# Kernel tuning notes

Measured on AMD Instinct MI355X. Metric: run time of the kernel, lower is better.

Reference implementation:

```python
import jax, jax.numpy as jnp
import numpy as np

N_NODES = 100000
N_EDGES = 1600000
C_IN, C_HID, C_OUT = 128, 64, 32


def setup_inputs() -> dict:
    key = jax.random.key(0)
    kx, ke, kw1, kw2 = jax.random.split(key, 4)
    x = jax.random.normal(kx, (N_NODES, C_IN), dtype=jnp.float32)
    edge_index = jax.random.randint(ke, (2, N_EDGES), 0, N_NODES, dtype=jnp.int64)
    # Glorot-ish init for the two GCNConv linear weights; PyG GCNConv bias inits to zero.
    W1 = jax.random.normal(kw1, (C_IN, C_HID), dtype=jnp.float32) / np.sqrt(C_IN)
    b1 = jnp.zeros((C_HID,), dtype=jnp.float32)
    W2 = jax.random.normal(kw2, (C_HID, C_OUT), dtype=jnp.float32) / np.sqrt(C_HID)
    b2 = jnp.zeros((C_OUT,), dtype=jnp.float32)
    return {"x": x, "edge_index": edge_index, "W1": W1, "b1": b1, "W2": W2, "b2": b2}


def _gcn_conv(x, W, b, src, dst, num_nodes):
    """PyG GCNConv: add self-loops, symmetric norm D^-1/2 A D^-1/2, linear, aggregate, bias."""
    xw = x @ W  # [N, out]
    # degree at destination, including the self-loop contribution of 1 per node
    deg = jnp.zeros((num_nodes,), xw.dtype).at[dst].add(1.0) + 1.0
    dinv = jax.lax.rsqrt(deg)  # deg >= 1 thanks to self-loops
    norm = dinv[src] * dinv[dst]  # [E]
    # scatter-add messages from source nodes into destination nodes
    out = jnp.zeros_like(xw).at[dst].add(norm[:, None] * xw[src])
    # self-loop term: norm_ii = dinv[i]^2
    out = out + (dinv * dinv)[:, None] * xw
    return out + b


def reference(x, edge_index, W1, b1, W2, b2):
    src, dst = edge_index[0], edge_index[1]
    h = _gcn_conv(x, W1, b1, src, dst, N_NODES)
    h = jax.nn.relu(h)
    # Dropout(0.1) is identity in eval mode (deterministic reference)
    out = _gcn_conv(h, W2, b2, src, dst, N_NODES)
    return out
```

## Files before the change

### kernel.cpp

```cpp
#include <hip/hip_runtime.h>
#include <hip/hip_bf16.h>


#define C_IN  128
#define C_HID 64
#define C_OUT 32
#define BK_SHIFT 10
#define BK_NODES (1 << BK_SHIFT)
#define BK_MAXB  128
#define EPB 2048

typedef unsigned short ushort_t;
typedef __attribute__((ext_vector_type(8))) short bf16x8;
typedef __attribute__((ext_vector_type(4))) float f32x4;

__device__ inline ushort_t f2bf(float f) {
    __hip_bfloat16 b = __float2bfloat16(f);
    return *reinterpret_cast<ushort_t*>(&b);
}
__device__ inline float bflo(unsigned int v) { return __uint_as_float(v << 16); }
__device__ inline float bfhi(unsigned int v) { return __uint_as_float(v & 0xffff0000u); }


__global__ void zero_bcur(int* __restrict__ bcur, int nb) {
    int i = threadIdx.x;
    if (i < nb) bcur[i] = 0;
}

__global__ __launch_bounds__(256) void bucket_edges(
        const int* __restrict__ src, const int* __restrict__ dst,
        int* __restrict__ bcur, unsigned int* __restrict__ bucketed,
        int cap, int E, int nb) {
    __shared__ unsigned int stage[EPB];
    __shared__ unsigned char bkt[EPB];
    __shared__ int cnt[BK_MAXB];
    __shared__ int lofs[BK_MAXB];
    __shared__ int base[BK_MAXB];
    int tid = threadIdx.x;
    for (int i = tid; i < nb; i += 256) cnt[i] = 0;
    __syncthreads();
    int e0 = blockIdx.x * EPB;
    int myb[8]; int myr[8]; unsigned int mys[8];
    #pragma unroll
    for (int i = 0; i < 8; ++i) {
        int e = e0 + i * 256 + tid;
        if (e < E) {
            int d = dst[e];
            int s = src[e];
            int b = d >> BK_SHIFT;
            myb[i] = b;
            mys[i] = (unsigned int)s | ((unsigned int)(d & (BK_NODES - 1)) << 17);
            myr[i] = atomicAdd(&cnt[b], 1);
        } else myb[i] = -1;
    }
    __syncthreads();
    if (tid < 64) {
        int b0 = 2 * tid, b1 = 2 * tid + 1;
        int c0 = (b0 < nb) ? cnt[b0] : 0;
        int c1 = (b1 < nb) ? cnt[b1] : 0;
        int p = c0 + c1;
        int s = p;
        #pragma unroll
        for (int off = 1; off < 64; off <<= 1) {
            int t = __shfl_up(s, off, 64);
            if (tid >= off) s += t;
        }
        if (b0 < nb) lofs[b0] = s - p;
        if (b1 < nb) lofs[b1] = s - c1;
    }
    __syncthreads();
    #pragma unroll
    for (int i = 0; i < 8; ++i) {
        if (myb[i] >= 0) {
            int p = lofs[myb[i]] + myr[i];
            stage[p] = mys[i];
            bkt[p] = (unsigned char)myb[i];
        }
    }
    for (int i = tid; i < nb; i += 256)
        base[i] = atomicAdd(&bcur[i], cnt[i]);
    __syncthreads();
    int total = min(EPB, E - e0);
    for (int p = tid; p < total; p += 256) {
        int b = bkt[p];
        int di = base[b] + (p - lofs[b]);
        if (di < cap)
            bucketed[(size_t)b * cap + di] = stage[p];
    }
}

__global__ __launch_bounds__(1024) void fill_csr_fused(
        const unsigned int* __restrict__ bucketed, const int* __restrict__ bcur,
        int* __restrict__ offsets, float* __restrict__ dinv,
        int* __restrict__ csr_src, int cap, int nb, int n) {
    __shared__ int hist[BK_NODES];
    __shared__ int wsum[16];
    __shared__ int sEb[BK_MAXB + 1];
    __shared__ int sW[2];
    int tid = threadIdx.x, lane = tid & 63, wid = tid >> 6;
    int b = blockIdx.x;
    int v128 = 0, s128 = 0;
    if (tid < 128) {
        v128 = (tid < nb) ? min(bcur[tid], cap) : 0;
        s128 = v128;
        #pragma unroll
        for (int off = 1; off < 64; off <<= 1) {
            int t = __shfl_up(s128, off, 64);
            if (lane >= off) s128 += t;
        }
        if (lane == 63) sW[wid] = s128;
    }
    __syncthreads();
    if (tid < 128) {
        int incl = s128 + ((wid == 1) ? sW[0] : 0);
        sEb[tid] = incl - v128;
        if (tid == nb - 1) sEb[nb] = incl;
    }
    hist[tid] = 0;
    __syncthreads();
    int eb = sEb[b];
    int cnt = sEb[b + 1] - eb;
    if (b == 0 && tid == 0) offsets[n] = sEb[nb];
    int node0 = b << BK_SHIFT;
    int nn = min(BK_NODES, n - node0);
    const unsigned int* bp = bucketed + (size_t)b * cap;
    for (int e = tid; e < cnt; e += 1024)
        atomicAdd(&hist[bp[e] >> 17], 1);
    __syncthreads();
    int v = hist[tid];
    int s = v;
    #pragma unroll
    for (int off = 1; off < 64; off <<= 1) {
        int t = __shfl_up(s, off, 64);
        if (lane >= off) s += t;
    }
    if (lane == 63) wsum[wid] = s;
    __syncthreads();
    if (wid == 0 && lane < 16) {
        int ws = wsum[lane];
        #pragma unroll
        for (int off = 1; off < 16; off <<= 1) {
            int t = __shfl_up(ws, off, 64);
            if (lane >= off) ws += t;
        }
        wsum[lane] = ws;
    }
    __syncthreads();
    int wpre = (wid > 0) ? wsum[wid - 1] : 0;
    int excl = wpre + s - v;
    if (tid < nn) {
        offsets[node0 + tid] = eb + excl;
        dinv[node0 + tid] = rsqrtf((float)v + 1.0f);
    }
    __syncthreads();
    hist[tid] = eb + excl;
    __syncthreads();
    for (int e = tid; e < cnt; e += 1024) {
        unsigned int u = bp[e];
        int pos = atomicAdd(&hist[u >> 17], 1);
        csr_src[pos] = (int)(u & 0x1FFFFu);
    }
}

__global__ void count_deg(const int* __restrict__ dst, int* __restrict__ deg, int E) {
    int idx = blockIdx.x * blockDim.x + threadIdx.x;
    int stride = gridDim.x * blockDim.x;
    for (int e = idx; e < E; e += stride)
        atomicAdd(&deg[dst[e]], 1);
}

__global__ void fill_csr(const int* __restrict__ src, const int* __restrict__ dst,
                         int* __restrict__ cursor, int* __restrict__ csr_src, int E) {
    int idx = blockIdx.x * blockDim.x + threadIdx.x;
    int stride = gridDim.x * blockDim.x;
    for (int e = idx; e < E; e += stride) {
        int pos = atomicAdd(&cursor[dst[e]], 1);
        csr_src[pos] = src[e];
    }
}

__global__ void scan_blocks(const int* __restrict__ deg, int* __restrict__ offsets,
                            int* __restrict__ bsums, float* __restrict__ dinv, int n) {
    __shared__ int wsum[16];
    int tid = threadIdx.x, lane = tid & 63, wid = tid >> 6;
    int i = blockIdx.x * 1024 + tid;
    int v = (i < n) ? deg[i] : 0;
    if (i < n) dinv[i] = rsqrtf((float)v + 1.0f);
    int s = v;
    #pragma unroll
    for (int off = 1; off < 64; off <<= 1) {
        int t = __shfl_up(s, off, 64);
        if (lane >= off) s += t;
    }
    if (lane == 63) wsum[wid] = s;
    __syncthreads();
    if (wid == 0 && lane < 16) {
        int ws = wsum[lane];
        #pragma unroll
        for (int off = 1; off < 16; off <<= 1) {
            int t = __shfl_up(ws, off, 64);
            if (lane >= off) ws += t;
        }
        wsum[lane] = ws;
        if (lane == 15) bsums[blockIdx.x] = ws;
    }
    __syncthreads();
    int wpre = (wid > 0) ? wsum[wid - 1] : 0;
    if (i < n) offsets[i] = wpre + s - v;
}

__global__ void scan_bsums(int* __restrict__ bsums, int nb) {
    __shared__ int wsum[16];
    int tid = threadIdx.x, lane = tid & 63, wid = tid >> 6;
    int v = (tid < nb) ? bsums[tid] : 0;
    int s = v;
    #pragma unroll
    for (int off = 1; off < 64; off <<= 1) {
        int t = __shfl_up(s, off, 64);
        if (lane >= off) s += t;
    }
    if (lane == 63) wsum[wid] = s;
    __syncthreads();
    if (wid == 0 && lane < 16) {
        int ws = wsum[lane];
        #pragma unroll
        for (int off = 1; off < 16; off <<= 1) {
            int t = __shfl_up(ws, off, 64);
            if (lane >= off) ws += t;
        }
        wsum[lane] = ws;
    }
    __syncthreads();
    int wpre = (wid > 0) ? wsum[wid - 1] : 0;
    if (tid < nb) bsums[tid] = wpre + s - v;
}

__global__ void scan_add(int* __restrict__ offsets, const int* __restrict__ bsums,
                         int n, int E) {
    int i = blockIdx.x * 1024 + threadIdx.x;
    if (i < n) offsets[i] += bsums[blockIdx.x];
    if (i == 0) offsets[n] = E;
}

__global__ __launch_bounds__(256) void gemm1_mfma(
        const float* __restrict__ x, const float* __restrict__ W1,
        const float* __restrict__ dinv, ushort_t* __restrict__ xws_bf, int n) {
    __shared__ ushort_t Xs[64 * 136];
    __shared__ ushort_t Wl[16 * 64 * 8];
    int tid = threadIdx.x;
    {
        const float4* Wv = reinterpret_cast<const float4*>(W1);
        #pragma unroll
        for (int p = 0; p < 8; ++p) {
            int idx = p * 256 + tid;
            float4 w = Wv[idx];
            int k = idx >> 4;
            int c0 = (idx & 15) * 4;
            ushort_t* d = &Wl[(k >> 3) * 512 + c0 * 8 + (k & 7)];
            d[0]  = f2bf(w.x);
            d[8]  = f2bf(w.y);
            d[16] = f2bf(w.z);
            d[24] = f2bf(w.w);
        }
    }
    int row0 = blockIdx.x * 64;
    {
        const float4* xv = reinterpret_cast<const float4*>(x + (size_t)row0 * C_IN);
        int maxv = min(64, n - row0) * (C_IN / 4);
        #pragma unroll
        for (int p = 0; p < 8; ++p) {
            int idx = p * 256 + tid;
            float4 v = (idx < maxv) ? xv[idx] : float4{0.f, 0.f, 0.f, 0.f};
            int row = idx >> 5, k4 = idx & 31;
            ushort4 pk;
            pk.x = f2bf(v.x); pk.y = f2bf(v.y); pk.z = f2bf(v.z); pk.w = f2bf(v.w);
            *reinterpret_cast<ushort4*>(&Xs[row * 136 + k4 * 4]) = pk;
        }
    }
    __syncthreads();
    int wid = tid >> 6, lane = tid & 63;
    int rbase = wid * 16;
    int l15 = lane & 15, kgrp = lane >> 4;
    f32x4 acc0 = {0.f, 0.f, 0.f, 0.f}, acc1 = acc0, acc2 = acc0, acc3 = acc0;
    #pragma unroll
    for (int kc = 0; kc < 4; ++kc) {
        bf16x8 a = *reinterpret_cast<const bf16x8*>(&Xs[(rbase + l15) * 136 + kc * 32 + kgrp * 8]);
        const ushort_t* wb = &Wl[(kc * 4 + kgrp) * 512 + l15 * 8];
        bf16x8 b0 = *reinterpret_cast<const bf16x8*>(wb);
        bf16x8 b1 = *reinterpret_cast<const bf16x8*>(wb + 128);
        bf16x8 b2 = *reinterpret_cast<const bf16x8*>(wb + 256);
        bf16x8 b3 = *reinterpret_cast<const bf16x8*>(wb + 384);
        acc0 = __builtin_amdgcn_mfma_f32_16x16x32_bf16(a, b0, acc0, 0, 0, 0);
        acc1 = __builtin_amdgcn_mfma_f32_16x16x32_bf16(a, b1, acc1, 0, 0, 0);
        acc2 = __builtin_amdgcn_mfma_f32_16x16x32_bf16(a, b2, acc2, 0, 0, 0);
        acc3 = __builtin_amdgcn_mfma_f32_16x16x32_bf16(a, b3, acc3, 0, 0, 0);
    }
    #pragma unroll
    for (int j = 0; j < 4; ++j) {
        int row = row0 + rbase + kgrp * 4 + j;
        if (row < n) {
            float di = dinv[row];
            ushort_t* o = &xws_bf[(size_t)row * C_HID + l15];
            o[0]  = f2bf(di * acc0[j]);
            o[16] = f2bf(di * acc1[j]);
            o[32] = f2bf(di * acc2[j]);
            o[48] = f2bf(di * acc3[j]);
        }
    }
}

__global__ __launch_bounds__(256) void gemm2_mfma(
        const ushort_t* __restrict__ h_bf, const float* __restrict__ W2,
        const float* __restrict__ dinv, ushort_t* __restrict__ xws2_bf, int n) {
    __shared__ ushort_t Hs[64 * 72];
    __shared__ ushort_t Wl[8 * 32 * 8];
    int tid = threadIdx.x;
    {
        const float4* Wv = reinterpret_cast<const float4*>(W2);
        #pragma unroll
        for (int p = 0; p < 2; ++p) {
            int idx = p * 256 + tid;
            float4 w = Wv[idx];
            int k = idx >> 3;
            int c0 = (idx & 7) * 4;
            ushort_t* d = &Wl[(k >> 3) * 256 + c0 * 8 + (k & 7)];
            d[0]  = f2bf(w.x);
            d[8]  = f2bf(w.y);
            d[16] = f2bf(w.z);
            d[24] = f2bf(w.w);
        }
    }
    int row0 = blockIdx.x * 64;
    {
        const uint4* hv = reinterpret_cast<const uint4*>(h_bf + (size_t)row0 * C_HID);
        int maxv = min(64, n - row0) * 8;
        #pragma unroll
        for (int p = 0; p < 2; ++p) {
            int idx = p * 256 + tid;
            uint4 v = (idx < maxv) ? hv[idx] : uint4{0u, 0u, 0u, 0u};
            int row = idx >> 3, c16 = idx & 7;
            *reinterpret_cast<uint4*>(&Hs[row * 72 + c16 * 8]) = v;
        }
    }
    __syncthreads();
    int wid = tid >> 6, lane = tid & 63;
    int rbase = wid * 16;
    int l15 = lane & 15, kgrp = lane >> 4;
    f32x4 acc0 = {0.f, 0.f, 0.f, 0.f}, acc1 = acc0;
    #pragma unroll
    for (int kc = 0; kc < 2; ++kc) {
        bf16x8 a = *reinterpret_cast<const bf16x8*>(&Hs[(rbase + l15) * 72 + kc * 32 + kgrp * 8]);
        const ushort_t* wb = &Wl[(kc * 4 + kgrp) * 256 + l15 * 8];
        bf16x8 b0 = *reinterpret_cast<const bf16x8*>(wb);
        bf16x8 b1 = *reinterpret_cast<const bf16x8*>(wb + 128);
        acc0 = __builtin_amdgcn_mfma_f32_16x16x32_bf16(a, b0, acc0, 0, 0, 0);
        acc1 = __builtin_amdgcn_mfma_f32_16x16x32_bf16(a, b1, acc1, 0, 0, 0);
    }
    #pragma unroll
    for (int j = 0; j < 4; ++j) {
        int row = row0 + rbase + kgrp * 4 + j;
        if (row < n) {
            float di = dinv[row];
            ushort_t* o = &xws2_bf[(size_t)row * C_OUT + l15];
            o[0]  = f2bf(di * acc0[j]);
            o[16] = f2bf(di * acc1[j]);
        }
    }
}


__global__ void agg1(const ushort_t* __restrict__ xws_bf, const float* __restrict__ dinv,
                     const int* __restrict__ offsets, const int* __restrict__ csr_src,
                     const float* __restrict__ b1, ushort_t* __restrict__ h_bf, int n) {
    int wid = threadIdx.x >> 6, lane = threadIdx.x & 63;
    int half = lane >> 5, c2 = lane & 31;
    const unsigned int* xu = reinterpret_cast<const unsigned int*>(xws_bf);
    float2 bb = *reinterpret_cast<const float2*>(&b1[2 * c2]);
    for (int base = (blockIdx.x * 4 + wid) * 2; base < n; base += gridDim.x * 8) {
        int i = base + half;
        if (i < n) {
            int beg = offsets[i], end = offsets[i + 1];
            float di = dinv[i];
            unsigned int sv = xu[(size_t)i * 32 + c2];
            float a0 = bflo(sv), a1 = bfhi(sv);
            int k = beg;
            for (; k + 8 <= end; k += 8) {
                int s0 = csr_src[k + 0];
                int s1 = csr_src[k + 1];
                int s2 = csr_src[k + 2];
                int s3 = csr_src[k + 3];
                int s4 = csr_src[k + 4];
                int s5 = csr_src[k + 5];
                int s6 = csr_src[k + 6];
                int s7 = csr_src[k + 7];
                unsigned int v0 = xu[(size_t)s0 * 32 + c2];
                unsigned int v1 = xu[(size_t)s1 * 32 + c2];
                unsigned int v2 = xu[(size_t)s2 * 32 + c2];
                unsigned int v3 = xu[(size_t)s3 * 32 + c2];
                unsigned int v4 = xu[(size_t)s4 * 32 + c2];
                unsigned int v5 = xu[(size_t)s5 * 32 + c2];
                unsigned int v6 = xu[(size_t)s6 * 32 + c2];
                unsigned int v7 = xu[(size_t)s7 * 32 + c2];
                a0 += ((bflo(v0) + bflo(v1)) + (bflo(v2) + bflo(v3)))
                    + ((bflo(v4) + bflo(v5)) + (bflo(v6) + bflo(v7)));
                a1 += ((bfhi(v0) + bfhi(v1)) + (bfhi(v2) + bfhi(v3)))
                    + ((bfhi(v4) + bfhi(v5)) + (bfhi(v6) + bfhi(v7)));
            }
            for (; k + 4 <= end; k += 4) {
                int s0 = csr_src[k + 0];
                int s1 = csr_src[k + 1];
                int s2 = csr_src[k + 2];
                int s3 = csr_src[k + 3];
                unsigned int v0 = xu[(size_t)s0 * 32 + c2];
                unsigned int v1 = xu[(size_t)s1 * 32 + c2];
                unsigned int v2 = xu[(size_t)s2 * 32 + c2];
                unsigned int v3 = xu[(size_t)s3 * 32 + c2];
                a0 += (bflo(v0) + bflo(v1)) + (bflo(v2) + bflo(v3));
                a1 += (bfhi(v0) + bfhi(v1)) + (bfhi(v2) + bfhi(v3));
            }
            for (; k < end; ++k) {
                int s = csr_src[k];
                unsigned int v = xu[(size_t)s * 32 + c2];
                a0 += bflo(v); a1 += bfhi(v);
            }
            float r0 = fmaxf(di * a0 + bb.x, 0.f);
            float r1 = fmaxf(di * a1 + bb.y, 0.f);
            unsigned int pk = (unsigned int)f2bf(r0) | ((unsigned int)f2bf(r1) << 16);
            *reinterpret_cast<unsigned int*>(&h_bf[(size_t)i * C_HID + 2 * c2]) = pk;
        }
    }
}

__global__ void agg2(const ushort_t* __restrict__ xws2_bf, const float* __restrict__ dinv,
                     const int* __restrict__ offsets, const int* __restrict__ csr_src,
                     const float* __restrict__ b2, float* __restrict__ out, int n) {
    int wid = threadIdx.x >> 6, lane = threadIdx.x & 63;
    int q = lane >> 4, c2 = lane & 15;
    const unsigned int* xu = reinterpret_cast<const unsigned int*>(xws2_bf);
    float2 bb = *reinterpret_cast<const float2*>(&b2[2 * c2]);
    for (int base = (blockIdx.x * 4 + wid) * 4; base < n; base += gridDim.x * 16) {
        int i = base + q;
        if (i < n) {
            int beg = offsets[i], end = offsets[i + 1];
            float di = dinv[i];
            unsigned int sv = xu[(size_t)i * 16 + c2];
            float a0 = bflo(sv), a1 = bfhi(sv);
            int k = beg;
            for (; k + 8 <= end; k += 8) {
                int s0 = csr_src[k + 0];
                int s1 = csr_src[k + 1];
                int s2 = csr_src[k + 2];
                int s3 = csr_src[k + 3];
                int s4 = csr_src[k + 4];
                int s5 = csr_src[k + 5];
                int s6 = csr_src[k + 6];
                int s7 = csr_src[k + 7];
                unsigned int v0 = xu[(size_t)s0 * 16 + c2];
                unsigned int v1 = xu[(size_t)s1 * 16 + c2];
                unsigned int v2 = xu[(size_t)s2 * 16 + c2];
                unsigned int v3 = xu[(size_t)s3 * 16 + c2];
                unsigned int v4 = xu[(size_t)s4 * 16 + c2];
                unsigned int v5 = xu[(size_t)s5 * 16 + c2];
                unsigned int v6 = xu[(size_t)s6 * 16 + c2];
                unsigned int v7 = xu[(size_t)s7 * 16 + c2];
                a0 += ((bflo(v0) + bflo(v1)) + (bflo(v2) + bflo(v3)))
                    + ((bflo(v4) + bflo(v5)) + (bflo(v6) + bflo(v7)));
                a1 += ((bfhi(v0) + bfhi(v1)) + (bfhi(v2) + bfhi(v3)))
                    + ((bfhi(v4) + bfhi(v5)) + (bfhi(v6) + bfhi(v7)));
            }
            for (; k + 4 <= end; k += 4) {
                int s0 = csr_src[k + 0];
                int s1 = csr_src[k + 1];
                int s2 = csr_src[k + 2];
                int s3 = csr_src[k + 3];
                unsigned int v0 = xu[(size_t)s0 * 16 + c2];
                unsigned int v1 = xu[(size_t)s1 * 16 + c2];
                unsigned int v2 = xu[(size_t)s2 * 16 + c2];
                unsigned int v3 = xu[(size_t)s3 * 16 + c2];
                a0 += (bflo(v0) + bflo(v1)) + (bflo(v2) + bflo(v3));
                a1 += (bfhi(v0) + bfhi(v1)) + (bfhi(v2) + bfhi(v3));
            }
            for (; k < end; ++k) {
                int s = csr_src[k];
                unsigned int v = xu[(size_t)s * 16 + c2];
                a0 += bflo(v); a1 += bfhi(v);
            }
            float2 r;
            r.x = di * a0 + bb.x;
            r.y = di * a1 + bb.y;
            *reinterpret_cast<float2*>(&out[(size_t)i * C_OUT + 2 * c2]) = r;
        }
    }
}

extern "C" void kernel_launch(void* const* d_in, const int* in_sizes, int n_in,
                              void* d_out, int out_size, void* d_ws, size_t ws_size,
                              hipStream_t stream) {
    const float* x  = (const float*)d_in[0];
    const int*   ei = (const int*)d_in[1];
    const float* W1 = (const float*)d_in[2];
    const float* b1 = (const float*)d_in[3];
    const float* W2 = (const float*)d_in[4];
    const float* b2 = (const float*)d_in[5];
    float* out = (float*)d_out;

    const int N = in_sizes[0] / C_IN;
    const int E = in_sizes[1] / 2;
    const int* src = ei;
    const int* dst = ei + E;

    const int NB = (N + BK_NODES - 1) >> BK_SHIFT;
    const int CAP = (2 * (E / NB) + 1023) & ~1023;

    char* ws = (char*)d_ws;
    size_t off = 0;
    auto alloc = [&](size_t bytes) { char* p = ws + off; off += (bytes + 255) & ~(size_t)255; return p; };
    ushort_t* xw_bf  = (ushort_t*)alloc((size_t)N * C_HID * 2);
    ushort_t* h_bf   = (ushort_t*)alloc((size_t)N * C_HID * 2);
    int*   deg     = (int*)alloc((size_t)N * 4);
    float* dinv    = (float*)alloc((size_t)N * 4);
    int*   offsets = (int*)alloc((size_t)(N + 1) * 4);
    int*   cursor  = (int*)alloc((size_t)N * 4);
    int*   csr_src = (int*)alloc((size_t)E * 4);
    int*   bsums   = (int*)alloc(4096);
    int*   bcur    = (int*)alloc((size_t)BK_MAXB * 4);
    unsigned int* bucketed = (unsigned int*)alloc((size_t)NB * CAP * 4);
    bool use_bucket = (off <= ws_size) && (NB <= BK_MAXB) && (N < (1 << 17));

    const int nb1024 = (N + 1023) / 1024;

    if (use_bucket) {
        zero_bcur<<<1, 128, 0, stream>>>(bcur, NB);
        bucket_edges<<<(E + EPB - 1) / EPB, 256, 0, stream>>>(
            src, dst, bcur, bucketed, CAP, E, NB);
        fill_csr_fused<<<NB, 1024, 0, stream>>>(bucketed, bcur, offsets, dinv,
                                                csr_src, CAP, NB, N);
    } else {
        hipMemsetAsync(deg, 0, (size_t)N * 4, stream);
        count_deg<<<2048, 256, 0, stream>>>(dst, deg, E);
        scan_blocks<<<nb1024, 1024, 0, stream>>>(deg, offsets, bsums, dinv, N);
        scan_bsums<<<1, 1024, 0, stream>>>(bsums, nb1024);
        scan_add<<<nb1024, 1024, 0, stream>>>(offsets, bsums, N, E);
        hipMemcpyAsync(cursor, offsets, (size_t)N * 4, hipMemcpyDeviceToDevice, stream);
        fill_csr<<<2048, 256, 0, stream>>>(src, dst, cursor, csr_src, E);
    }

    gemm1_mfma<<<(N + 63) / 64, 256, 0, stream>>>(x, W1, dinv, xw_bf, N);
    agg1<<<2048, 256, 0, stream>>>(xw_bf, dinv, offsets, csr_src, b1, h_bf, N);
    gemm2_mfma<<<(N + 63) / 64, 256, 0, stream>>>(h_bf, W2, dinv, xw_bf, N);
    agg2<<<2048, 256, 0, stream>>>(xw_bf, dinv, offsets, csr_src, b2, out, N);
}
```

Measured before the change: 132.6 us.

## Privatize per-wave bucket counters and deepen gather unrolling in aggregation

The edge-bucketing kernel now keeps a separate shared-memory bucket histogram per wavefront, cutting LDS atomic contention, and adds a two-level prefix scan to combine the per-wave counts into offsets. The first aggregation kernel gains a 16-wide unrolled gather loop so more independent loads are in flight per node. Both aggregation kernels restructure their 8-wide loop into array-based unrolled loads with sequential accumulation, which changes floating-point summation order. The scan contains a __syncthreads inside divergent branches, which is risky, and the wider unroll raises register pressure.

```diff
diff --git a/kernel.cpp b/kernel.cpp
--- a/kernel.cpp
+++ b/kernel.cpp
@@ -33,11 +33,15 @@
         int cap, int E, int nb) {
     __shared__ unsigned int stage[EPB];
     __shared__ unsigned char bkt[EPB];
-    __shared__ int cnt[BK_MAXB];
+    __shared__ int cnt[4][BK_MAXB];
+    __shared__ int wofs[4][BK_MAXB];
     __shared__ int lofs[BK_MAXB];
     __shared__ int base[BK_MAXB];
-    int tid = threadIdx.x;
-    for (int i = tid; i < nb; i += 256) cnt[i] = 0;
+    __shared__ int tot[BK_MAXB];
+    int tid = threadIdx.x, wid4 = tid >> 6;
+    #pragma unroll
+    for (int w = 0; w < 4; ++w)
+        for (int i = tid; i < nb; i += 256) cnt[w][i] = 0;
     __syncthreads();
     int e0 = blockIdx.x * EPB;
     int myb[8]; int myr[8]; unsigned int mys[8];
@@ -50,35 +54,48 @@
             int b = d >> BK_SHIFT;
             myb[i] = b;
             mys[i] = (unsigned int)s | ((unsigned int)(d & (BK_NODES - 1)) << 17);
-            myr[i] = atomicAdd(&cnt[b], 1);
+            myr[i] = atomicAdd(&cnt[wid4][b], 1);
         } else myb[i] = -1;
     }
     __syncthreads();
-    if (tid < 64) {
-        int b0 = 2 * tid, b1 = 2 * tid + 1;
-        int c0 = (b0 < nb) ? cnt[b0] : 0;
-        int c1 = (b1 < nb) ? cnt[b1] : 0;
-        int p = c0 + c1;
-        int s = p;
+    if (tid < 128) {
+        int b = tid;
+        int c0 = cnt[0][b], c1 = cnt[1][b], c2 = cnt[2][b], c3 = cnt[3][b];
+        tot[b] = c0 + c1 + c2 + c3;
+        wofs[0][b] = 0;
+        wofs[1][b] = c0;
+        wofs[2][b] = c0 + c1;
+        wofs[3][b] = c0 + c1 + c2;
+    }
+    __syncthreads();
+    if (tid < 128) {
+        int lane = tid & 63, w = tid >> 6;
+        int v = (tid < nb) ? tot[tid] : 0;
+        int s = v;
         #pragma unroll
         for (int off = 1; off < 64; off <<= 1) {
             int t = __shfl_up(s, off, 64);
-            if (tid >= off) s += t;
-        }
-        if (b0 < nb) lofs[b0] = s - p;
-        if (b1 < nb) lofs[b1] = s - c1;
+            if (lane >= off) s += t;
+        }
+        if (lane == 63) base[w] = s;
+        __syncthreads();
+        int incl = s + ((w == 1) ? base[0] : 0);
+        if (tid < nb) lofs[tid] = incl - v;
+    } else {
+        __syncthreads();
     }
     __syncthreads();
     #pragma unroll
     for (int i = 0; i < 8; ++i) {
         if (myb[i] >= 0) {
-            int p = lofs[myb[i]] + myr[i];
+            int b = myb[i];
+            int p = lofs[b] + wofs[wid4][b] + myr[i];
             stage[p] = mys[i];
-            bkt[p] = (unsigned char)myb[i];
+            bkt[p] = (unsigned char)b;
         }
     }
     for (int i = tid; i < nb; i += 256)
-        base[i] = atomicAdd(&bcur[i], cnt[i]);
+        base[i] = atomicAdd(&bcur[i], tot[i]);
     __syncthreads();
     int total = min(EPB, E - e0);
     for (int p = tid; p < total; p += 256) {
@@ -384,27 +401,27 @@
             unsigned int sv = xu[(size_t)i * 32 + c2];
             float a0 = bflo(sv), a1 = bfhi(sv);
             int k = beg;
+            for (; k + 16 <= end; k += 16) {
+                int si[16];
+                unsigned int vv[16];
+                #pragma unroll
+                for (int t = 0; t < 16; ++t) si[t] = csr_src[k + t];
+                #pragma unroll
+                for (int t = 0; t < 16; ++t) vv[t] = xu[(size_t)si[t] * 32 + c2];
+                float l0 = 0.f, h0 = 0.f;
+                #pragma unroll
+                for (int t = 0; t < 16; ++t) { l0 += bflo(vv[t]); h0 += bfhi(vv[t]); }
+                a0 += l0; a1 += h0;
+            }
             for (; k + 8 <= end; k += 8) {
-                int s0 = csr_src[k + 0];
-                int s1 = csr_src[k + 1];
-                int s2 = csr_src[k + 2];
-                int s3 = csr_src[k + 3];
-                int s4 = csr_src[k + 4];
-                int s5 = csr_src[k + 5];
-                int s6 = csr_src[k + 6];
-                int s7 = csr_src[k + 7];
-                unsigned int v0 = xu[(size_t)s0 * 32 + c2];
-                unsigned int v1 = xu[(size_t)s1 * 32 + c2];
-                unsigned int v2 = xu[(size_t)s2 * 32 + c2];
-                unsigned int v3 = xu[(size_t)s3 * 32 + c2];
-                unsigned int v4 = xu[(size_t)s4 * 32 + c2];
-                unsigned int v5 = xu[(size_t)s5 * 32 + c2];
-                unsigned int v6 = xu[(size_t)s6 * 32 + c2];
-                unsigned int v7 = xu[(size_t)s7 * 32 + c2];
-                a0 += ((bflo(v0) + bflo(v1)) + (bflo(v2) + bflo(v3)))
-                    + ((bflo(v4) + bflo(v5)) + (bflo(v6) + bflo(v7)));
-                a1 += ((bfhi(v0) + bfhi(v1)) + (bfhi(v2) + bfhi(v3)))
-                    + ((bfhi(v4) + bfhi(v5)) + (bfhi(v6) + bfhi(v7)));
+                int si[8];
+                unsigned int vv[8];
+                #pragma unroll
+                for (int t = 0; t < 8; ++t) si[t] = csr_src[k + t];
+                #pragma unroll
+                for (int t = 0; t < 8; ++t) vv[t] = xu[(size_t)si[t] * 32 + c2];
+                #pragma unroll
+                for (int t = 0; t < 8; ++t) { a0 += bflo(vv[t]); a1 += bfhi(vv[t]); }
             }
             for (; k + 4 <= end; k += 4) {
                 int s0 = csr_src[k + 0];
@@ -447,26 +464,14 @@
             float a0 = bflo(sv), a1 = bfhi(sv);
             int k = beg;
             for (; k + 8 <= end; k += 8) {
-                int s0 = csr_src[k + 0];
-                int s1 = csr_src[k + 1];
-                int s2 = csr_src[k + 2];
-                int s3 = csr_src[k + 3];
-                int s4 = csr_src[k + 4];
-                int s5 = csr_src[k + 5];
-                int s6 = csr_src[k + 6];
-                int s7 = csr_src[k + 7];
-                unsigned int v0 = xu[(size_t)s0 * 16 + c2];
-                unsigned int v1 = xu[(size_t)s1 * 16 + c2];
-                unsigned int v2 = xu[(size_t)s2 * 16 + c2];
-                unsigned int v3 = xu[(size_t)s3 * 16 + c2];
-                unsigned int v4 = xu[(size_t)s4 * 16 + c2];
-                unsigned int v5 = xu[(size_t)s5 * 16 + c2];
-                unsigned int v6 = xu[(size_t)s6 * 16 + c2];
-                unsigned int v7 = xu[(size_t)s7 * 16 + c2];
-                a0 += ((bflo(v0) + bflo(v1)) + (bflo(v2) + bflo(v3)))
-                    + ((bflo(v4) + bflo(v5)) + (bflo(v6) + bflo(v7)));
-                a1 += ((bfhi(v0) + bfhi(v1)) + (bfhi(v2) + bfhi(v3)))
-                    + ((bfhi(v4) + bfhi(v5)) + (bfhi(v6) + bfhi(v7)));
+                int si[8];
+                unsigned int vv[8];
+                #pragma unroll
+                for (int t = 0; t < 8; ++t) si[t] = csr_src[k + t];
+                #pragma unroll
+                for (int t = 0; t < 8; ++t) vv[t] = xu[(size_t)si[t] * 16 + c2];
+                #pragma unroll
+                for (int t = 0; t < 8; ++t) { a0 += bflo(vv[t]); a1 += bfhi(vv[t]); }
             }
             for (; k + 4 <= end; k += 4) {
                 int s0 = csr_src[k + 0];
```

Result: no change. 133.2 us (+0.4%).
